# Performance work log

Measured on AMD Instinct MI355X. Metric: run time of the kernel, lower is better.

## Reference

```python
import jax, jax.numpy as jnp
import numpy as np

N = 100_000   # nodes
E = 1_600_000 # edges (COO, directed as given)
D = 128       # input feature dim
H = 128       # hidden dim
L = 3         # layers


def setup_inputs() -> dict:
    key = jax.random.key(0)
    ks = jax.random.split(key, 2 + 2 * L)
    x = jax.random.normal(ks[0], (N, D), dtype=jnp.float32)
    edge_index = jax.random.randint(ks[1], (2, E), 0, N, dtype=jnp.int32)
    inp = {"x": x, "edge_index": edge_index}
    dims = [(D, H), (H, H), (H, H)]
    for i, (fi, fo) in enumerate(dims):
        scale = 1.0 / np.sqrt(fi)
        inp[f"W{i}"] = jax.random.uniform(ks[2 + 2 * i], (fi, fo), jnp.float32, -scale, scale)
        inp[f"b{i}"] = jax.random.uniform(ks[3 + 2 * i], (fo,), jnp.float32, -scale, scale)
    return inp


def reference(x, edge_index, W0, b0, W1, b1, W2, b2):
    n = x.shape[0]
    src, dst = edge_index[0], edge_index[1]
    # GCNConv default: add self-loops, symmetric D^{-1/2}(A+I)D^{-1/2} normalization
    loop = jnp.arange(n, dtype=edge_index.dtype)
    src = jnp.concatenate([src, loop])
    dst = jnp.concatenate([dst, loop])
    ones = jnp.ones(src.shape[0], dtype=x.dtype)
    deg = jax.ops.segment_sum(ones, dst, num_segments=n)          # [N]
    dinv = jnp.where(deg > 0, jax.lax.rsqrt(deg), 0.0)            # deg^{-1/2}, inf->0
    norm = dinv[src] * dinv[dst]                                  # [E+N]

    def gcn_conv(h, W, b):
        h = h @ W                                  # linear transform first (PyG order)
        msg = h[src] * norm[:, None]               # gather + scale, [E+N, H]
        return jax.ops.segment_sum(msg, dst, num_segments=n) + b

    for W, b in ((W0, b0), (W1, b1), (W2, b2)):
        x = jax.nn.relu(gcn_conv(x, W, b))
    return x
```

## Files before the change

### kernel.cpp

```cpp
#include <hip/hip_runtime.h>
#include <hip/hip_bf16.h>

#define TPB 256

typedef short s8v __attribute__((ext_vector_type(8)));
typedef float f4v __attribute__((ext_vector_type(4)));
typedef _Float16 h8v __attribute__((ext_vector_type(8)));

#define PB 128
#define BSHIFT 10
#define BSPAN 1024
#define PCHUNK 4096
#define WBLK 192

__device__ __forceinline__ unsigned short bf16_rne(float v) {
    unsigned int u = __float_as_uint(v);
    u += 0x7fffu + ((u >> 16) & 1u);
    return (unsigned short)(u >> 16);
}
__device__ __forceinline__ void split_bf16(float v, unsigned short& hi, unsigned short& lo) {
    hi = bf16_rne(v);
    float hf = __uint_as_float((unsigned int)hi << 16);
    lo = bf16_rne(v - hf);
}


__global__ __launch_bounds__(256) void bhist_wsplit_kernel(const int* __restrict__ dst, int E,
                                                           int* __restrict__ bsize,
                                                           const float* __restrict__ W0,
                                                           const float* __restrict__ W1,
                                                           const float* __restrict__ W2,
                                                           unsigned short* __restrict__ Whi,
                                                           unsigned short* __restrict__ Wlo) {
    __shared__ int h[PB];
    int t = threadIdx.x;
    if (blockIdx.x < WBLK) {
        int idx0 = blockIdx.x * 256 + t;
        if (idx0 < 3 * 16384) {
            int layer = idx0 >> 14;
            int e = idx0 & 16383;
            int k = e >> 7, ncol = e & 127;
            const float* W = (layer == 0) ? W0 : (layer == 1) ? W1 : W2;
            unsigned short hi, lo;
            split_bf16(W[e], hi, lo);
            int ct = ncol >> 4;
            int lane = (((k >> 3) & 3) << 4) | (ncol & 15);
            int kki = k >> 5;
            int j = k & 7;
            int oidx = layer * 16384 + (((ct * 4 + kki) * 64 + lane) * 8 + j);
            Whi[oidx] = hi; Wlo[oidx] = lo;
        }
        return;
    }
    int blk = blockIdx.x - WBLK;
    int nblk = gridDim.x - WBLK;
    if (t < PB) h[t] = 0;
    __syncthreads();
    for (int e = blk * 256 + t; e < E; e += nblk * 256)
        atomicAdd(&h[dst[e] >> BSHIFT], 1);
    __syncthreads();
    if (t < PB && h[t] > 0) atomicAdd(&bsize[t], h[t]);
}

__global__ void bscan_kernel(const int* __restrict__ bsize, int* __restrict__ bbase,
                             int* __restrict__ bcursor, int* __restrict__ row, int n, int E) {
    __shared__ int wtot[2];
    int t = threadIdx.x;
    int sz = bsize[t];
    int lane = t & 63, wid = t >> 6;
    int v = sz;
    for (int off = 1; off < 64; off <<= 1) {
        int u = __shfl_up(v, off);
        if (lane >= off) v += u;
    }
    if (lane == 63) wtot[wid] = v;
    __syncthreads();
    if (wid == 1) v += wtot[0];
    bbase[t + 1] = v;
    bcursor[t] = v - sz;
    if (t == 0) { bbase[0] = 0; row[n] = E; }
}

__global__ __launch_bounds__(256) void partition_kernel(const int* __restrict__ src,
                                                        const int* __restrict__ dst, int E,
                                                        int* __restrict__ bcursor,
                                                        int2* __restrict__ part) {
    __shared__ int h[PB];
    __shared__ int gofs[PB];
    int t = threadIdx.x;
    long base = (long)blockIdx.x * PCHUNK;
    int cnt = (int)min((long)PCHUNK, (long)E - base);

    if (t < PB) h[t] = 0;
    __syncthreads();
    for (int j = t; j < cnt; j += 256)
        atomicAdd(&h[dst[base + j] >> BSHIFT], 1);
    __syncthreads();
    if (t < PB) gofs[t] = (h[t] > 0) ? atomicAdd(&bcursor[t], h[t]) : 0;
    __syncthreads();
    if (t < PB) h[t] = 0;
    __syncthreads();
    for (int j = t; j < cnt; j += 256) {
        int s = src[base + j], d = dst[base + j];
        int b = d >> BSHIFT;
        int idx = atomicAdd(&h[b], 1);
        part[(long)gofs[b] + idx] = make_int2(s, d);
    }
}

__global__ __launch_bounds__(1024) void csr_kernel(const int2* __restrict__ part,
                                                   const int* __restrict__ bbase,
                                                   int* __restrict__ row, float* __restrict__ dinv,
                                                   int* __restrict__ esrc, int n) {
    __shared__ int deg[BSPAN];
    __shared__ int lrow[BSPAN];
    __shared__ int cur[BSPAN];
    __shared__ int wsum[16];
    int b = blockIdx.x;
    int n0 = b << BSHIFT;
    int nn = min(BSPAN, n - n0);
    if (nn <= 0) return;
    int e0 = bbase[b], e1 = bbase[b + 1];
    int t = threadIdx.x;

    deg[t] = 0;
    __syncthreads();
    for (int e = e0 + t; e < e1; e += 1024)
        atomicAdd(&deg[part[e].y - n0], 1);
    __syncthreads();

    int a = deg[t];
    int lane = t & 63, wid = t >> 6;
    int v = a;
    for (int off = 1; off < 64; off <<= 1) {
        int u = __shfl_up(v, off);
        if (lane >= off) v += u;
    }
    if (lane == 63) wsum[wid] = v;
    __syncthreads();
    if (wid == 0 && lane < 16) {
        int w = wsum[lane];
        for (int off = 1; off < 16; off <<= 1) {
            int u = __shfl_up(w, off);
            if (lane >= off) w += u;
        }
        wsum[lane] = w;
    }
    __syncthreads();
    int excl = v - a + ((wid > 0) ? wsum[wid - 1] : 0);
    lrow[t] = excl;
    cur[t] = 0;
    if (t < nn) {
        row[n0 + t] = e0 + excl;
        dinv[n0 + t] = rsqrtf((float)(deg[t] + 1));
    }
    __syncthreads();

    for (int e = e0 + t; e < e1; e += 1024) {
        int2 p = part[e];
        int d = p.y - n0;
        int idx = atomicAdd(&cur[d], 1);
        esrc[e0 + lrow[d] + idx] = p.x;
    }
}


__global__ __launch_bounds__(256, 3) void gemm0_mfma(const float* __restrict__ Xf,
                                                     const unsigned short* __restrict__ Whs,
                                                     const unsigned short* __restrict__ Wls,
                                                     _Float16* __restrict__ Ch, int n) {
    __shared__ _Float16 Oh[128 * 136];
    int t = threadIdx.x;
    int wave = t >> 6, lane = t & 63;
    int ch = wave & 1, rh = wave >> 1;
    int lm = lane & 15, q = lane >> 4;
    long row0 = (long)blockIdx.x * 128 + rh * 64;

    const s8v* Wh8 = (const s8v*)Whs;
    const s8v* Wl8 = (const s8v*)Wls;

    f4v acc[4][4];
#pragma unroll
    for (int rt = 0; rt < 4; rt++)
#pragma unroll
        for (int ct = 0; ct < 4; ct++) acc[rt][ct] = (f4v)0.0f;

#pragma unroll
    for (int kki = 0; kki < 4; kki++) {
        s8v bh[4], bl[4];
#pragma unroll
        for (int ct = 0; ct < 4; ct++) {
            int idx = (((ch * 4 + ct) * 4 + kki) * 64) + lane;
            bh[ct] = Wh8[idx];
            bl[ct] = Wl8[idx];
        }
        s8v ah[4], al[4];
#pragma unroll
        for (int rt = 0; rt < 4; rt++) {
            long r = row0 + rt * 16 + lm;
            long rr = (r < n) ? r : (n - 1);
            const float4* xf4 = (const float4*)(Xf + rr * 128 + kki * 32 + q * 8);
            float4 u0 = xf4[0], u1 = xf4[1];
            float uf[8] = {u0.x, u0.y, u0.z, u0.w, u1.x, u1.y, u1.z, u1.w};
            s8v hv, lv;
#pragma unroll
            for (int j = 0; j < 8; j++) {
                unsigned short hh, ll;
                split_bf16(uf[j], hh, ll);
                hv[j] = (short)hh; lv[j] = (short)ll;
            }
            ah[rt] = hv; al[rt] = lv;
        }
#pragma unroll
        for (int rt = 0; rt < 4; rt++)
#pragma unroll
            for (int ct = 0; ct < 4; ct++) {
                acc[rt][ct] = __builtin_amdgcn_mfma_f32_16x16x32_bf16(ah[rt], bh[ct], acc[rt][ct], 0, 0, 0);
                acc[rt][ct] = __builtin_amdgcn_mfma_f32_16x16x32_bf16(ah[rt], bl[ct], acc[rt][ct], 0, 0, 0);
                acc[rt][ct] = __builtin_amdgcn_mfma_f32_16x16x32_bf16(al[rt], bh[ct], acc[rt][ct], 0, 0, 0);
            }
    }

#pragma unroll
    for (int rt = 0; rt < 4; rt++)
#pragma unroll
        for (int reg = 0; reg < 4; reg++) {
            int lr = rh * 64 + rt * 16 + q * 4 + reg;
#pragma unroll
            for (int ct = 0; ct < 4; ct++)
                Oh[lr * 136 + ch * 64 + ct * 16 + lm] = (_Float16)acc[rt][ct][reg];
        }
    __syncthreads();

    long rowb = (long)blockIdx.x * 128;
    int lr = t >> 1;
    int cb = (t & 1) * 64;
    if (rowb + lr < n) {
        const uint4* s = (const uint4*)&Oh[lr * 136 + cb];
        uint4* d = (uint4*)&Ch[(rowb + lr) * 128 + cb];
#pragma unroll
        for (int u = 0; u < 8; u++) d[u] = s[u];
    }
}


__global__ __launch_bounds__(256) void fused_kernel(const h8v* __restrict__ hIn,
                                                    const float* __restrict__ dinv,
                                                    const int* __restrict__ row,
                                                    const int* __restrict__ esrc,
                                                    const float* __restrict__ bias,
                                                    const unsigned short* __restrict__ Whs,
                                                    const unsigned short* __restrict__ Wls,
                                                    _Float16* __restrict__ hOut, int n) {
    __shared__ float As[16 * 132];
    int t = threadIdx.x;
    int g = t >> 4, lane = t & 15;
    long i = (long)blockIdx.x * 16 + g;

    float r[8];
    if (i < n) {
        float di = dinv[i];
        float s2 = di * di;
        h8v self = hIn[i * 16 + lane];
        float acc[8];
#pragma unroll
        for (int k = 0; k < 8; k++) acc[k] = (float)self[k] * s2;

        int e0 = row[i], e1 = row[i + 1];
        int e = e0;
        for (; e + 4 <= e1; e += 4) {
            int s0 = esrc[e + 0];
            int s1 = esrc[e + 1];
            int s2i = esrc[e + 2];
            int s3 = esrc[e + 3];
            h8v v0 = hIn[(size_t)s0 * 16 + lane];
            h8v v1 = hIn[(size_t)s1 * 16 + lane];
            h8v v2 = hIn[(size_t)s2i * 16 + lane];
            h8v v3 = hIn[(size_t)s3 * 16 + lane];
            float w0 = dinv[s0] * di;
            float w1 = dinv[s1] * di;
            float w2 = dinv[s2i] * di;
            float w3 = dinv[s3] * di;
#pragma unroll
            for (int k = 0; k < 8; k++)
                acc[k] += w0 * (float)v0[k] + w1 * (float)v1[k] + w2 * (float)v2[k] + w3 * (float)v3[k];
        }
        for (; e < e1; ++e) {
            int s = esrc[e];
            h8v v = hIn[(size_t)s * 16 + lane];
            float w = dinv[s] * di;
#pragma unroll
            for (int k = 0; k < 8; k++) acc[k] += w * (float)v[k];
        }

        const float4* b4 = (const float4*)(bias + lane * 8);
        float4 bA = b4[0], bB = b4[1];
        r[0] = fmaxf(acc[0] + bA.x, 0.f); r[1] = fmaxf(acc[1] + bA.y, 0.f);
        r[2] = fmaxf(acc[2] + bA.z, 0.f); r[3] = fmaxf(acc[3] + bA.w, 0.f);
        r[4] = fmaxf(acc[4] + bB.x, 0.f); r[5] = fmaxf(acc[5] + bB.y, 0.f);
        r[6] = fmaxf(acc[6] + bB.z, 0.f); r[7] = fmaxf(acc[7] + bB.w, 0.f);
    } else {
#pragma unroll
        for (int k = 0; k < 8; k++) r[k] = 0.f;
    }

    float* dstA = &As[g * 132 + lane * 8];
    *(float4*)dstA = make_float4(r[0], r[1], r[2], r[3]);
    *(float4*)(dstA + 4) = make_float4(r[4], r[5], r[6], r[7]);
    __syncthreads();

    int w = t >> 6, l64 = t & 63;
    int lm = l64 & 15, q = l64 >> 4;

    const s8v* Wh8 = (const s8v*)Whs;
    const s8v* Wl8 = (const s8v*)Wls;
    s8v Bh[2][4], Bl[2][4];
#pragma unroll
    for (int c = 0; c < 2; c++)
#pragma unroll
        for (int kki = 0; kki < 4; kki++) {
            int idx = (((w * 2 + c) * 4 + kki) * 64) + l64;
            Bh[c][kki] = Wh8[idx];
            Bl[c][kki] = Wl8[idx];
        }

    f4v acc2[2];
    acc2[0] = (f4v)0.0f; acc2[1] = (f4v)0.0f;

#pragma unroll
    for (int kki = 0; kki < 4; kki++) {
        const float* ap = &As[lm * 132 + kki * 32 + q * 8];
        float4 u0 = *(const float4*)ap;
        float4 u1 = *(const float4*)(ap + 4);
        float uf[8] = {u0.x, u0.y, u0.z, u0.w, u1.x, u1.y, u1.z, u1.w};
        s8v hv, lv;
#pragma unroll
        for (int j = 0; j < 8; j++) {
            unsigned short hh, ll;
            split_bf16(uf[j], hh, ll);
            hv[j] = (short)hh; lv[j] = (short)ll;
        }
#pragma unroll
        for (int c = 0; c < 2; c++) {
            acc2[c] = __builtin_amdgcn_mfma_f32_16x16x32_bf16(hv, Bh[c][kki], acc2[c], 0, 0, 0);
            acc2[c] = __builtin_amdgcn_mfma_f32_16x16x32_bf16(hv, Bl[c][kki], acc2[c], 0, 0, 0);
            acc2[c] = __builtin_amdgcn_mfma_f32_16x16x32_bf16(lv, Bh[c][kki], acc2[c], 0, 0, 0);
        }
    }
    __syncthreads();

    _Float16* Oh = (_Float16*)As;
#pragma unroll
    for (int c = 0; c < 2; c++)
#pragma unroll
        for (int reg = 0; reg < 4; reg++)
            Oh[(q * 4 + reg) * 136 + (w * 2 + c) * 16 + lm] = (_Float16)acc2[c][reg];
    __syncthreads();

    long gi = (long)blockIdx.x * 16 + (t >> 4);
    if (gi < n) {
        uint4 v = *(const uint4*)&Oh[(t >> 4) * 136 + (t & 15) * 8];
        *(uint4*)&hOut[gi * 128 + (size_t)(t & 15) * 8] = v;
    }
}


__global__ __launch_bounds__(256) void agg_final(const h8v* __restrict__ hH,
                                                 const float* __restrict__ dinv,
                                                 const int* __restrict__ row,
                                                 const int* __restrict__ esrc,
                                                 const float* __restrict__ bias,
                                                 float* __restrict__ out, int n) {
    int g    = threadIdx.x >> 4;
    int lane = threadIdx.x & 15;
    int i = blockIdx.x * 16 + g;
    if (i >= n) return;

    float di = dinv[i];
    float s2 = di * di;

    h8v self = hH[(size_t)i * 16 + lane];
    float acc[8];
#pragma unroll
    for (int k = 0; k < 8; k++) acc[k] = (float)self[k] * s2;

    int e0 = row[i], e1 = row[i + 1];
    int e = e0;
    for (; e + 4 <= e1; e += 4) {
        int s0 = esrc[e + 0];
        int s1 = esrc[e + 1];
        int s2i = esrc[e + 2];
        int s3 = esrc[e + 3];
        h8v v0 = hH[(size_t)s0 * 16 + lane];
        h8v v1 = hH[(size_t)s1 * 16 + lane];
        h8v v2 = hH[(size_t)s2i * 16 + lane];
        h8v v3 = hH[(size_t)s3 * 16 + lane];
        float w0 = dinv[s0] * di;
        float w1 = dinv[s1] * di;
        float w2 = dinv[s2i] * di;
        float w3 = dinv[s3] * di;
#pragma unroll
        for (int k = 0; k < 8; k++)
            acc[k] += w0 * (float)v0[k] + w1 * (float)v1[k] + w2 * (float)v2[k] + w3 * (float)v3[k];
    }
    for (; e < e1; ++e) {
        int s = esrc[e];
        h8v v = hH[(size_t)s * 16 + lane];
        float w = dinv[s] * di;
#pragma unroll
        for (int k = 0; k < 8; k++) acc[k] += w * (float)v[k];
    }

    const float4* b4 = (const float4*)(bias + lane * 8);
    float4 bA = b4[0], bB = b4[1];
    float4* o4 = (float4*)(out + (size_t)i * 128 + lane * 8);
    o4[0] = make_float4(fmaxf(acc[0] + bA.x, 0.f), fmaxf(acc[1] + bA.y, 0.f),
                        fmaxf(acc[2] + bA.z, 0.f), fmaxf(acc[3] + bA.w, 0.f));
    o4[1] = make_float4(fmaxf(acc[4] + bB.x, 0.f), fmaxf(acc[5] + bB.y, 0.f),
                        fmaxf(acc[6] + bB.z, 0.f), fmaxf(acc[7] + bB.w, 0.f));
}


extern "C" void kernel_launch(void* const* d_in, const int* in_sizes, int n_in,
                              void* d_out, int out_size, void* d_ws, size_t ws_size,
                              hipStream_t stream) {
    const float* x  = (const float*)d_in[0];
    const int*   ei = (const int*)d_in[1];
    const float* W0 = (const float*)d_in[2];
    const float* b0 = (const float*)d_in[3];
    const float* W1 = (const float*)d_in[4];
    const float* b1 = (const float*)d_in[5];
    const float* W2 = (const float*)d_in[6];
    const float* b2 = (const float*)d_in[7];

    const int H = 128;
    int n = in_sizes[0] / H;
    int E = in_sizes[1] / 2;
    const int* srcp = ei;
    const int* dstp = ei + E;

    int gemm_blocks = (n + 127) / 128;
    long npad = (long)gemm_blocks * 128;
    int nbuck = (n + BSPAN - 1) >> BSHIFT;

    char* p = (char*)d_ws;
    auto alloc = [&](size_t bytes) {
        void* r = (void*)p;
        p += (bytes + 255) & ~(size_t)255;
        return r;
    };
    _Float16* bufH0 = (_Float16*)alloc((size_t)npad * H * 2);
    _Float16* bufH1 = (_Float16*)alloc((size_t)npad * H * 2);
    unsigned short* Whs = (unsigned short*)alloc(3 * 16384 * 2);
    unsigned short* Wls = (unsigned short*)alloc(3 * 16384 * 2);
    float* dinv  = (float*)alloc((size_t)n * sizeof(float));
    int*  row    = (int*)alloc((size_t)(n + 1) * sizeof(int));
    int*  bsize  = (int*)alloc(PB * sizeof(int));
    int*  bbase  = (int*)alloc((PB + 1) * sizeof(int));
    int*  bcursor= (int*)alloc(PB * sizeof(int));
    int2* part   = (int2*)alloc((size_t)E * sizeof(int2));
    int*  esrc   = (int*)alloc((size_t)E * sizeof(int));

    hipMemsetAsync(bsize, 0, PB * sizeof(int), stream);

    bhist_wsplit_kernel<<<WBLK + 1024, 256, 0, stream>>>(dstp, E, bsize, W0, W1, W2, Whs, Wls);
    bscan_kernel<<<1, PB, 0, stream>>>(bsize, bbase, bcursor, row, n, E);
    partition_kernel<<<(E + PCHUNK - 1) / PCHUNK, 256, 0, stream>>>(srcp, dstp, E, bcursor, part);
    csr_kernel<<<nbuck, 1024, 0, stream>>>(part, bbase, row, dinv, esrc, n);

    float* out = (float*)d_out;
    int node_blocks = (n + 15) / 16;

    gemm0_mfma<<<gemm_blocks, 256, 0, stream>>>(x, Whs, Wls, bufH0, n);
    fused_kernel<<<node_blocks, 256, 0, stream>>>((const h8v*)bufH0, dinv, row, esrc, b0,
                                                  Whs + 16384, Wls + 16384, bufH1, n);
    fused_kernel<<<node_blocks, 256, 0, stream>>>((const h8v*)bufH1, dinv, row, esrc, b1,
                                                  Whs + 32768, Wls + 32768, bufH0, n);
    agg_final<<<node_blocks, 256, 0, stream>>>((const h8v*)bufH0, dinv, row, esrc, b2, out, n);
}
```

Before: 410.5 us.

## Prescale features by dinv to drop per-edge normalization gathers, unroll by eight

The source-side dinv factor is folded into the stored features: the layer-0 GEMM scales input rows by dinv, and each fused layer multiplies its output by dinv before the next transform. Aggregation then becomes a plain sum of gathered rows, which removes the per-edge dinv[src] gather and multiply. The edge loop is unrolled to eight, and a zero padding row (index n) is used as the target of masked tail loads so there is no scalar remainder loop. The cost is two extra memsets for the padding rows, plus slightly different fp16 rounding because prescaled values are stored.

```diff
diff --git a/kernel.cpp b/kernel.cpp
--- a/kernel.cpp
+++ b/kernel.cpp
@@ -168,6 +168,7 @@
 __global__ __launch_bounds__(256, 3) void gemm0_mfma(const float* __restrict__ Xf,
                                                      const unsigned short* __restrict__ Whs,
                                                      const unsigned short* __restrict__ Wls,
+                                                     const float* __restrict__ dinv,
                                                      _Float16* __restrict__ Ch, int n) {
     __shared__ _Float16 Oh[128 * 136];
     int t = threadIdx.x;
@@ -179,6 +180,14 @@
     const s8v* Wh8 = (const s8v*)Whs;
     const s8v* Wl8 = (const s8v*)Wls;
 
+    float scs[4];
+#pragma unroll
+    for (int rt = 0; rt < 4; rt++) {
+        long r = row0 + rt * 16 + lm;
+        long rc = (r < n) ? r : (n - 1);
+        scs[rt] = dinv[rc];
+    }
+
     f4v acc[4][4];
 #pragma unroll
     for (int rt = 0; rt < 4; rt++)
@@ -202,11 +211,12 @@
             const float4* xf4 = (const float4*)(Xf + rr * 128 + kki * 32 + q * 8);
             float4 u0 = xf4[0], u1 = xf4[1];
             float uf[8] = {u0.x, u0.y, u0.z, u0.w, u1.x, u1.y, u1.z, u1.w};
+            float sc = scs[rt];
             s8v hv, lv;
 #pragma unroll
             for (int j = 0; j < 8; j++) {
                 unsigned short hh, ll;
-                split_bf16(uf[j], hh, ll);
+                split_bf16(uf[j] * sc, hh, ll);
                 hv[j] = (short)hh; lv[j] = (short)ll;
             }
             ah[rt] = hv; al[rt] = lv;
@@ -251,7 +261,7 @@
                                                     const float* __restrict__ bias,
                                                     const unsigned short* __restrict__ Whs,
                                                     const unsigned short* __restrict__ Wls,
-                                                    _Float16* __restrict__ hOut, int n) {
+                                                    _Float16* __restrict__ hOut, int n, int nzr) {
     __shared__ float As[16 * 132];
     int t = threadIdx.x;
     int g = t >> 4, lane = t & 15;
@@ -260,45 +270,51 @@
     float r[8];
     if (i < n) {
         float di = dinv[i];
-        float s2 = di * di;
         h8v self = hIn[i * 16 + lane];
         float acc[8];
 #pragma unroll
-        for (int k = 0; k < 8; k++) acc[k] = (float)self[k] * s2;
+        for (int k = 0; k < 8; k++) acc[k] = (float)self[k];
 
         int e0 = row[i], e1 = row[i + 1];
+        int deg = e1 - e0;
+        int eFull = e1 - (deg & 7);
         int e = e0;
-        for (; e + 4 <= e1; e += 4) {
-            int s0 = esrc[e + 0];
-            int s1 = esrc[e + 1];
-            int s2i = esrc[e + 2];
-            int s3 = esrc[e + 3];
-            h8v v0 = hIn[(size_t)s0 * 16 + lane];
-            h8v v1 = hIn[(size_t)s1 * 16 + lane];
-            h8v v2 = hIn[(size_t)s2i * 16 + lane];
-            h8v v3 = hIn[(size_t)s3 * 16 + lane];
-            float w0 = dinv[s0] * di;
-            float w1 = dinv[s1] * di;
-            float w2 = dinv[s2i] * di;
-            float w3 = dinv[s3] * di;
-#pragma unroll
-            for (int k = 0; k < 8; k++)
-                acc[k] += w0 * (float)v0[k] + w1 * (float)v1[k] + w2 * (float)v2[k] + w3 * (float)v3[k];
-        }
-        for (; e < e1; ++e) {
-            int s = esrc[e];
-            h8v v = hIn[(size_t)s * 16 + lane];
-            float w = dinv[s] * di;
-#pragma unroll
-            for (int k = 0; k < 8; k++) acc[k] += w * (float)v[k];
+        for (; e < eFull; e += 8) {
+            int s[8];
+#pragma unroll
+            for (int j = 0; j < 8; j++) s[j] = esrc[e + j];
+            h8v v[8];
+#pragma unroll
+            for (int j = 0; j < 8; j++) v[j] = hIn[(size_t)s[j] * 16 + lane];
+#pragma unroll
+            for (int j = 0; j < 8; j++)
+#pragma unroll
+                for (int k = 0; k < 8; k++) acc[k] += (float)v[j][k];
+        }
+        if (e < e1) {
+            int s[8];
+#pragma unroll
+            for (int j = 0; j < 8; j++) {
+                int idx = e + j;
+                int ic = (idx < e1) ? idx : (e1 - 1);
+                int sv = esrc[ic];
+                s[j] = (idx < e1) ? sv : nzr;
+            }
+            h8v v[8];
+#pragma unroll
+            for (int j = 0; j < 8; j++) v[j] = hIn[(size_t)s[j] * 16 + lane];
+#pragma unroll
+            for (int j = 0; j < 8; j++)
+#pragma unroll
+                for (int k = 0; k < 8; k++) acc[k] += (float)v[j][k];
         }
 
         const float4* b4 = (const float4*)(bias + lane * 8);
         float4 bA = b4[0], bB = b4[1];
-        r[0] = fmaxf(acc[0] + bA.x, 0.f); r[1] = fmaxf(acc[1] + bA.y, 0.f);
-        r[2] = fmaxf(acc[2] + bA.z, 0.f); r[3] = fmaxf(acc[3] + bA.w, 0.f);
-        r[4] = fmaxf(acc[4] + bB.x, 0.f); r[5] = fmaxf(acc[5] + bB.y, 0.f);
-        r[6] = fmaxf(acc[6] + bB.z, 0.f); r[7] = fmaxf(acc[7] + bB.w, 0.f);
+        float bb[8] = {bA.x, bA.y, bA.z, bA.w, bB.x, bB.y, bB.z, bB.w};
+#pragma unroll
+        for (int k = 0; k < 8; k++)
+            r[k] = di * fmaxf(di * acc[k] + bb[k], 0.f);
     } else {
 #pragma unroll
         for (int k = 0; k < 8; k++) r[k] = 0.f;
@@ -370,54 +386,59 @@
                                                  const int* __restrict__ row,
                                                  const int* __restrict__ esrc,
                                                  const float* __restrict__ bias,
-                                                 float* __restrict__ out, int n) {
+                                                 float* __restrict__ out, int n, int nzr) {
     int g    = threadIdx.x >> 4;
     int lane = threadIdx.x & 15;
     int i = blockIdx.x * 16 + g;
     if (i >= n) return;
 
     float di = dinv[i];
-    float s2 = di * di;
-
     h8v self = hH[(size_t)i * 16 + lane];
     float acc[8];
 #pragma unroll
-    for (int k = 0; k < 8; k++) acc[k] = (float)self[k] * s2;
+    for (int k = 0; k < 8; k++) acc[k] = (float)self[k];
 
     int e0 = row[i], e1 = row[i + 1];
+    int deg = e1 - e0;
+    int eFull = e1 - (deg & 7);
     int e = e0;
-    for (; e + 4 <= e1; e += 4) {
-        int s0 = esrc[e + 0];
-        int s1 = esrc[e + 1];
-        int s2i = esrc[e + 2];
-        int s3 = esrc[e + 3];
-        h8v v0 = hH[(size_t)s0 * 16 + lane];
-        h8v v1 = hH[(size_t)s1 * 16 + lane];
-        h8v v2 = hH[(size_t)s2i * 16 + lane];
-        h8v v3 = hH[(size_t)s3 * 16 + lane];
-        float w0 = dinv[s0] * di;
-        float w1 = dinv[s1] * di;
-        float w2 = dinv[s2i] * di;
-        float w3 = dinv[s3] * di;
-#pragma unroll
-        for (int k = 0; k < 8; k++)
-            acc[k] += w0 * (float)v0[k] + w1 * (float)v1[k] + w2 * (float)v2[k] + w3 * (float)v3[k];
-    }
-    for (; e < e1; ++e) {
-        int s = esrc[e];
-        h8v v = hH[(size_t)s * 16 + lane];
-        float w = dinv[s] * di;
-#pragma unroll
-        for (int k = 0; k < 8; k++) acc[k] += w * (float)v[k];
+    for (; e < eFull; e += 8) {
+        int s[8];
+#pragma unroll
+        for (int j = 0; j < 8; j++) s[j] = esrc[e + j];
+        h8v v[8];
+#pragma unroll
+        for (int j = 0; j < 8; j++) v[j] = hH[(size_t)s[j] * 16 + lane];
+#pragma unroll
+        for (int j = 0; j < 8; j++)
+#pragma unroll
+            for (int k = 0; k < 8; k++) acc[k] += (float)v[j][k];
+    }
+    if (e < e1) {
+        int s[8];
+#pragma unroll
+        for (int j = 0; j < 8; j++) {
+            int idx = e + j;
+            int ic = (idx < e1) ? idx : (e1 - 1);
+            int sv = esrc[ic];
+            s[j] = (idx < e1) ? sv : nzr;
+        }
+        h8v v[8];
+#pragma unroll
+        for (int j = 0; j < 8; j++) v[j] = hH[(size_t)s[j] * 16 + lane];
+#pragma unroll
+        for (int j = 0; j < 8; j++)
+#pragma unroll
+            for (int k = 0; k < 8; k++) acc[k] += (float)v[j][k];
     }
 
     const float4* b4 = (const float4*)(bias + lane * 8);
     float4 bA = b4[0], bB = b4[1];
     float4* o4 = (float4*)(out + (size_t)i * 128 + lane * 8);
-    o4[0] = make_float4(fmaxf(acc[0] + bA.x, 0.f), fmaxf(acc[1] + bA.y, 0.f),
-                        fmaxf(acc[2] + bA.z, 0.f), fmaxf(acc[3] + bA.w, 0.f));
-    o4[1] = make_float4(fmaxf(acc[4] + bB.x, 0.f), fmaxf(acc[5] + bB.y, 0.f),
-                        fmaxf(acc[6] + bB.z, 0.f), fmaxf(acc[7] + bB.w, 0.f));
+    o4[0] = make_float4(fmaxf(di * acc[0] + bA.x, 0.f), fmaxf(di * acc[1] + bA.y, 0.f),
+                        fmaxf(di * acc[2] + bA.z, 0.f), fmaxf(di * acc[3] + bA.w, 0.f));
+    o4[1] = make_float4(fmaxf(di * acc[4] + bB.x, 0.f), fmaxf(di * acc[5] + bB.y, 0.f),
+                        fmaxf(di * acc[6] + bB.z, 0.f), fmaxf(di * acc[7] + bB.w, 0.f));
 }
 
 
@@ -441,6 +462,7 @@
 
     int gemm_blocks = (n + 127) / 128;
     long npad = (long)gemm_blocks * 128;
+    long rowsAlloc = npad + 128;
     int nbuck = (n + BSPAN - 1) >> BSHIFT;
 
     char* p = (char*)d_ws;
@@ -449,8 +471,8 @@
         p += (bytes + 255) & ~(size_t)255;
         return r;
     };
-    _Float16* bufH0 = (_Float16*)alloc((size_t)npad * H * 2);
-    _Float16* bufH1 = (_Float16*)alloc((size_t)npad * H * 2);
+    _Float16* bufH0 = (_Float16*)alloc((size_t)rowsAlloc * H * 2);
+    _Float16* bufH1 = (_Float16*)alloc((size_t)rowsAlloc * H * 2);
     unsigned short* Whs = (unsigned short*)alloc(3 * 16384 * 2);
     unsigned short* Wls = (unsigned short*)alloc(3 * 16384 * 2);
     float* dinv  = (float*)alloc((size_t)n * sizeof(float));
@@ -462,6 +484,8 @@
     int*  esrc   = (int*)alloc((size_t)E * sizeof(int));
 
     hipMemsetAsync(bsize, 0, PB * sizeof(int), stream);
+    hipMemsetAsync(bufH0 + (size_t)n * H, 0, (size_t)(rowsAlloc - n) * H * 2, stream);
+    hipMemsetAsync(bufH1 + (size_t)n * H, 0, (size_t)(rowsAlloc - n) * H * 2, stream);
 
     bhist_wsplit_kernel<<<WBLK + 1024, 256, 0, stream>>>(dstp, E, bsize, W0, W1, W2, Whs, Wls);
     bscan_kernel<<<1, PB, 0, stream>>>(bsize, bbase, bcursor, row, n, E);
@@ -471,10 +495,10 @@
     float* out = (float*)d_out;
     int node_blocks = (n + 15) / 16;
 
-    gemm0_mfma<<<gemm_blocks, 256, 0, stream>>>(x, Whs, Wls, bufH0, n);
+    gemm0_mfma<<<gemm_blocks, 256, 0, stream>>>(x, Whs, Wls, dinv, bufH0, n);
     fused_kernel<<<node_blocks, 256, 0, stream>>>((const h8v*)bufH0, dinv, row, esrc, b0,
-                                                  Whs + 16384, Wls + 16384, bufH1, n);
+                                                  Whs + 16384, Wls + 16384, bufH1, n, n);
     fused_kernel<<<node_blocks, 256, 0, stream>>>((const h8v*)bufH1, dinv, row, esrc, b1,
-                                                  Whs + 32768, Wls + 32768, bufH0, n);
-    agg_final<<<node_blocks, 256, 0, stream>>>((const h8v*)bufH0, dinv, row, esrc, b2, out, n);
-}
+                                                  Whs + 32768, Wls + 32768, bufH0, n, n);
+    agg_final<<<node_blocks, 256, 0, stream>>>((const h8v*)bufH0, dinv, row, esrc, b2, out, n, n);
+}
```

Result: faster. 398.0 us (-3.1%).
